# Performance work log

Measured on AMD Instinct MI355X. Metric: run time of the kernel, lower is better.

The kernel has to match this reference:

```python
import jax, jax.numpy as jnp
import numpy as np

TEMP = 0.5  # init temperature
EPS = 1e-12  # F.normalize eps


def setup_inputs() -> dict:
    key = jax.random.key(0)
    k1, k2 = jax.random.split(key)
    batch_embedding = jax.random.normal(k1, (4096, 256), dtype=jnp.float32)
    labels = jax.random.randint(k2, (4096,), 0, 512, dtype=jnp.int64)
    return {"batch_embedding": batch_embedding, "labels": labels}


def reference(batch_embedding, labels):
    n = labels.shape[0]
    dt = batch_embedding.dtype
    # row-normalize; cosine_similarity of normalized rows == norm @ norm.T
    nrm = jnp.linalg.norm(batch_embedding, axis=1, keepdims=True)
    norm = batch_embedding / jnp.maximum(nrm, EPS)
    sim = norm @ norm.T  # [n, n]
    mask = (labels[:, None] == labels[None, :]).astype(dt)  # same-label pairs (incl. diagonal)
    eye = jnp.eye(n, dtype=dt)
    exp_sim = jnp.exp(sim / TEMP) * (1.0 - eye)  # zero diagonal
    pos = mask * exp_sim
    neg_sum = jnp.sum(exp_sim - pos, axis=1)  # per-row negative sum
    ratio = pos / (pos + neg_sum[:, None])
    loss_mat = -jnp.log((1.0 - mask) + ratio + eye)
    nnz = jnp.count_nonzero(loss_mat).astype(dt)
    return jnp.sum(loss_mat) / nnz
```

## Files before the change

kernel.cpp:

```cpp
#include <hip/hip_runtime.h>
#include <hip/hip_bf16.h>


#define N_ROWS 4096
#define K_DIM  256

typedef __attribute__((ext_vector_type(8))) short short8;
typedef __attribute__((ext_vector_type(4))) float float4v;
typedef __attribute__((ext_vector_type(4))) float f4;

#define PK_OFF    0
#define PART_OFF  (N_ROWS * K_DIM * 2)
#define PART_SZ   (5 * 32 * N_ROWS)
#define ACC_OFF   (PART_OFF + PART_SZ * 4)

__global__ void normalize_kernel(const float* __restrict__ emb,
                                 short* __restrict__ pk,
                                 float* __restrict__ acc) {
    int tile = blockIdx.x, t = threadIdx.x;
    __shared__ float lds[16 * 256];
    __shared__ float sc[16];
    const f4* src = (const f4*)(emb + tile * 16 * 256);
    f4* dst4 = (f4*)lds;
    #pragma unroll
    for (int it = 0; it < 4; ++it) dst4[t + 256 * it] = src[t + 256 * it];
    __syncthreads();
    int wave = t >> 6, lane = t & 63;
    int row = wave * 4 + (lane >> 4);
    float s = 0.f;
    #pragma unroll
    for (int m = 0; m < 16; ++m) {
        float x = lds[row * 256 + (lane & 15) + 16 * m];
        s += x * x;
    }
    s += __shfl_xor(s, 1); s += __shfl_xor(s, 2);
    s += __shfl_xor(s, 4); s += __shfl_xor(s, 8);
    float scale = 1.0f / fmaxf(sqrtf(s), 1e-12f);
    if ((lane & 15) == 0) sc[row] = scale;
    __syncthreads();
    short out[16];
    #pragma unroll
    for (int u = 0; u < 16; ++u) {
        int p = t * 16 + u;
        int j = p & 7, r16 = (p >> 3) & 15, quad = (p >> 7) & 3, c = p >> 9;
        int k = quad * 8 + c * 32 + j;
        float v = lds[r16 * 256 + k] * sc[r16];
        __hip_bfloat16 b = __float2bfloat16(v);
        out[u] = *(short*)&b;
    }
    short* dst = pk + tile * 4096 + t * 16;
    *(short8*)dst = *(short8*)out;
    *(short8*)(dst + 8) = *(short8*)(out + 8);
    if (tile == 0 && t < 2) acc[t] = 0.0f;
}

__global__ __launch_bounds__(512, 4)
void negsum_kernel(const short* __restrict__ pk,
                   const int* __restrict__ labels,
                   float* __restrict__ part) {
    __shared__ short bs[8 * 4096];
    __shared__ int   labS[128];
    int t = threadIdx.x;
    int w = t >> 6, lane = t & 63;
    int row16 = lane & 15, quad = lane >> 4;
    int J = blockIdx.x & 31;
    int igroup = blockIdx.x >> 5;

    {
        const short8* src = (const short8*)(pk + J * 32768);
        short8* dst = (short8*)bs;
        #pragma unroll
        for (int it = 0; it < 8; ++it)
            dst[t + it * 512] = src[t + it * 512];
        if (t < 128) labS[t] = labels[J * 128 + t];
    }
    __syncthreads();

    short8 af[2][8];
    int istrip0 = igroup * 16 + w * 2;
    #pragma unroll
    for (int s = 0; s < 2; ++s) {
        const short* ap = pk + ((istrip0 + s) << 12) + lane * 8;
        #pragma unroll
        for (int c = 0; c < 8; ++c)
            af[s][c] = *(const short8*)(ap + (c << 9));
    }
    int irow[2][4], labi[2][4];
    #pragma unroll
    for (int s = 0; s < 2; ++s)
        #pragma unroll
        for (int r = 0; r < 4; ++r) {
            irow[s][r] = (istrip0 + s) * 16 + quad * 4 + r;
            labi[s][r] = labels[irow[s][r]];
        }

    float nacc[2][4] = {{0,0,0,0},{0,0,0,0}};
    float pe[2][4]   = {{0,0,0,0},{0,0,0,0}};
    float pe2[2][4]  = {{0,0,0,0},{0,0,0,0}};
    float ptt[2][4]  = {{0,0,0,0},{0,0,0,0}};
    float pc[2][4]   = {{0,0,0,0},{0,0,0,0}};

    for (int jt = 0; jt < 8; ++jt) {
        const short* bp = bs + (jt << 12) + lane * 8;
        float4v acc[2] = {{0.f,0.f,0.f,0.f},{0.f,0.f,0.f,0.f}};
        #pragma unroll
        for (int c = 0; c < 8; ++c) {
            short8 b = *(const short8*)(bp + (c << 9));
            acc[0] = __builtin_amdgcn_mfma_f32_16x16x32_bf16(af[0][c], b, acc[0], 0, 0, 0);
            acc[1] = __builtin_amdgcn_mfma_f32_16x16x32_bf16(af[1][c], b, acc[1], 0, 0, 0);
        }
        int j    = J * 128 + jt * 16 + row16;
        int labj = labS[jt * 16 + row16];
        #pragma unroll
        for (int s = 0; s < 2; ++s) {
            #pragma unroll
            for (int r = 0; r < 4; ++r) {
                float t2 = 2.0f * acc[s][r];
                float e  = __expf(t2);
                bool same = (labj == labi[s][r]);
                bool p    = same && (j != irow[s][r]);
                float m   = p ? 1.0f : 0.0f;
                nacc[s][r] += same ? 0.0f : e;
                pe[s][r]   = fmaf(m, e,      pe[s][r]);
                pe2[s][r]  = fmaf(m, e * e,  pe2[s][r]);
                ptt[s][r]  = fmaf(m, t2,     ptt[s][r]);
                pc[s][r]  += m;
            }
        }
    }

    #pragma unroll
    for (int s = 0; s < 2; ++s)
        #pragma unroll
        for (int r = 0; r < 4; ++r) {
            float v0 = nacc[s][r], v1 = pe[s][r], v2 = pe2[s][r];
            float v3 = ptt[s][r],  v4 = pc[s][r];
            #pragma unroll
            for (int m = 1; m < 16; m <<= 1) {
                v0 += __shfl_xor(v0, m); v1 += __shfl_xor(v1, m);
                v2 += __shfl_xor(v2, m); v3 += __shfl_xor(v3, m);
                v4 += __shfl_xor(v4, m);
            }
            if (row16 == 0) {
                int idx = J * N_ROWS + irow[s][r];
                part[0 * 32 * N_ROWS + idx] = v0;
                part[1 * 32 * N_ROWS + idx] = v1;
                part[2 * 32 * N_ROWS + idx] = v2;
                part[3 * 32 * N_ROWS + idx] = v3;
                part[4 * 32 * N_ROWS + idx] = v4;
            }
        }
}

__global__ void rowreduce_kernel(const float* __restrict__ part,
                                 float* __restrict__ acc) {
    int i = blockIdx.x * 256 + threadIdx.x;
    float n = 0.f, e1 = 0.f, e2 = 0.f, tt = 0.f, c = 0.f;
    for (int J = 0; J < 32; ++J) {
        int idx = J * N_ROWS + i;
        n  += part[0 * 32 * N_ROWS + idx];
        e1 += part[1 * 32 * N_ROWS + idx];
        e2 += part[2 * 32 * N_ROWS + idx];
        tt += part[3 * 32 * N_ROWS + idx];
        c  += part[4 * 32 * N_ROWS + idx];
    }
    float lsum = 0.f;
    if (c > 0.f) {
        float invn = 1.0f / n;
        lsum = c * logf(n) + e1 * invn - 0.5f * e2 * invn * invn - tt;
    }
    #pragma unroll
    for (int off = 32; off > 0; off >>= 1) {
        lsum += __shfl_down(lsum, off, 64);
        c    += __shfl_down(c,    off, 64);
    }
    __shared__ float sl[4], sc2[4];
    int wave = threadIdx.x >> 6, lane = threadIdx.x & 63;
    if (lane == 0) { sl[wave] = lsum; sc2[wave] = c; }
    __syncthreads();
    if (threadIdx.x == 0) {
        atomicAdd(&acc[0], sl[0] + sl[1] + sl[2] + sl[3]);
        atomicAdd(&acc[1], sc2[0] + sc2[1] + sc2[2] + sc2[3]);
    }
}

__global__ void div_kernel(const float* __restrict__ acc, float* __restrict__ out) {
    if (threadIdx.x == 0) out[0] = acc[0] / acc[1];
}

extern "C" void kernel_launch(void* const* d_in, const int* in_sizes, int n_in,
                              void* d_out, int out_size, void* d_ws, size_t ws_size,
                              hipStream_t stream) {
    const float* emb    = (const float*)d_in[0];
    const int*   labels = (const int*)d_in[1];
    float* out = (float*)d_out;
    char*  ws  = (char*)d_ws;

    short* pk   = (short*)(ws + PK_OFF);
    float* part = (float*)(ws + PART_OFF);
    float* acc  = (float*)(ws + ACC_OFF);

    normalize_kernel<<<N_ROWS / 16, 256, 0, stream>>>(emb, pk, acc);
    negsum_kernel<<<512, 512, 0, stream>>>(pk, labels, part);
    rowreduce_kernel<<<16, 256, 0, stream>>>(part, acc);
    div_kernel<<<1, 64, 0, stream>>>(acc, out);
}
```

Before: 83.16 us.

## Use per-wave 64x64 register tiles with direct global loads and column-wise reduction

The similarity kernel drops the LDS-staged B panel and instead has each wave compute a 64x64 output tile with 16 MFMA accumulators, loading A and B fragments straight from global memory. Partial sums are now reduced along the row axis per column, which uses the symmetry of the similarity matrix, and the loss drops the second-order e^2 correction term in favour of the exact pe/n form. This cuts the partial buffers from five to four and removes the block barrier, but it raises register pressure and relies on L2 for operand reuse instead of shared memory.

```diff
diff --git a/kernel.cpp b/kernel.cpp
--- a/kernel.cpp
+++ b/kernel.cpp
@@ -11,8 +11,7 @@
 
 #define PK_OFF    0
 #define PART_OFF  (N_ROWS * K_DIM * 2)
-#define PART_SZ   (5 * 32 * N_ROWS)
-#define ACC_OFF   (PART_OFF + PART_SZ * 4)
+#define ACC_OFF   (PART_OFF + 4 * 64 * N_ROWS * 4)
 
 __global__ void normalize_kernel(const float* __restrict__ emb,
                                  short* __restrict__ pk,
@@ -54,129 +53,114 @@
     if (tile == 0 && t < 2) acc[t] = 0.0f;
 }
 
-__global__ __launch_bounds__(512, 4)
+__global__ __launch_bounds__(256, 2)
 void negsum_kernel(const short* __restrict__ pk,
                    const int* __restrict__ labels,
                    float* __restrict__ part) {
-    __shared__ short bs[8 * 4096];
-    __shared__ int   labS[128];
-    int t = threadIdx.x;
-    int w = t >> 6, lane = t & 63;
-    int row16 = lane & 15, quad = lane >> 4;
-    int J = blockIdx.x & 31;
-    int igroup = blockIdx.x >> 5;
+    int w = threadIdx.x >> 6, lane = threadIdx.x & 63;
+    int lane16 = lane & 15, quad = lane >> 4;
+    int wid = blockIdx.x * 4 + w;
+    int i64 = wid >> 6, j64 = wid & 63;
+    int ibase = i64 * 64, jbase = j64 * 64;
 
-    {
-        const short8* src = (const short8*)(pk + J * 32768);
-        short8* dst = (short8*)bs;
+    int labi[16], labj[4];
+    #pragma unroll
+    for (int it = 0; it < 4; ++it)
         #pragma unroll
-        for (int it = 0; it < 8; ++it)
-            dst[t + it * 512] = src[t + it * 512];
-        if (t < 128) labS[t] = labels[J * 128 + t];
+        for (int r = 0; r < 4; ++r)
+            labi[it * 4 + r] = labels[ibase + it * 16 + quad * 4 + r];
+    #pragma unroll
+    for (int jt = 0; jt < 4; ++jt)
+        labj[jt] = labels[jbase + jt * 16 + lane16];
+
+    float4v acc[4][4];
+    #pragma unroll
+    for (int a = 0; a < 4; ++a)
+        #pragma unroll
+        for (int b = 0; b < 4; ++b)
+            acc[a][b] = (float4v){0.f, 0.f, 0.f, 0.f};
+
+    for (int c = 0; c < 8; ++c) {
+        short8 af[4], bf[4];
+        #pragma unroll
+        for (int it = 0; it < 4; ++it)
+            af[it] = *(const short8*)(pk + (((i64 * 4 + it) << 12) | (c << 9)) + lane * 8);
+        #pragma unroll
+        for (int jt = 0; jt < 4; ++jt)
+            bf[jt] = *(const short8*)(pk + (((j64 * 4 + jt) << 12) | (c << 9)) + lane * 8);
+        #pragma unroll
+        for (int it = 0; it < 4; ++it)
+            #pragma unroll
+            for (int jt = 0; jt < 4; ++jt)
+                acc[it][jt] = __builtin_amdgcn_mfma_f32_16x16x32_bf16(
+                    af[it], bf[jt], acc[it][jt], 0, 0, 0);
     }
-    __syncthreads();
 
-    short8 af[2][8];
-    int istrip0 = igroup * 16 + w * 2;
+    float ex[4] = {0,0,0,0}, pe[4] = {0,0,0,0};
+    float tt[4] = {0,0,0,0}, pc[4] = {0,0,0,0};
     #pragma unroll
-    for (int s = 0; s < 2; ++s) {
-        const short* ap = pk + ((istrip0 + s) << 12) + lane * 8;
+    for (int it = 0; it < 4; ++it) {
         #pragma unroll
-        for (int c = 0; c < 8; ++c)
-            af[s][c] = *(const short8*)(ap + (c << 9));
-    }
-    int irow[2][4], labi[2][4];
-    #pragma unroll
-    for (int s = 0; s < 2; ++s)
-        #pragma unroll
-        for (int r = 0; r < 4; ++r) {
-            irow[s][r] = (istrip0 + s) * 16 + quad * 4 + r;
-            labi[s][r] = labels[irow[s][r]];
-        }
-
-    float nacc[2][4] = {{0,0,0,0},{0,0,0,0}};
-    float pe[2][4]   = {{0,0,0,0},{0,0,0,0}};
-    float pe2[2][4]  = {{0,0,0,0},{0,0,0,0}};
-    float ptt[2][4]  = {{0,0,0,0},{0,0,0,0}};
-    float pc[2][4]   = {{0,0,0,0},{0,0,0,0}};
-
-    for (int jt = 0; jt < 8; ++jt) {
-        const short* bp = bs + (jt << 12) + lane * 8;
-        float4v acc[2] = {{0.f,0.f,0.f,0.f},{0.f,0.f,0.f,0.f}};
-        #pragma unroll
-        for (int c = 0; c < 8; ++c) {
-            short8 b = *(const short8*)(bp + (c << 9));
-            acc[0] = __builtin_amdgcn_mfma_f32_16x16x32_bf16(af[0][c], b, acc[0], 0, 0, 0);
-            acc[1] = __builtin_amdgcn_mfma_f32_16x16x32_bf16(af[1][c], b, acc[1], 0, 0, 0);
-        }
-        int j    = J * 128 + jt * 16 + row16;
-        int labj = labS[jt * 16 + row16];
-        #pragma unroll
-        for (int s = 0; s < 2; ++s) {
+        for (int jt = 0; jt < 4; ++jt) {
+            int j = jbase + jt * 16 + lane16;
             #pragma unroll
             for (int r = 0; r < 4; ++r) {
-                float t2 = 2.0f * acc[s][r];
+                int i = ibase + it * 16 + quad * 4 + r;
+                float t2 = 2.0f * acc[it][jt][r];
                 float e  = __expf(t2);
-                bool same = (labj == labi[s][r]);
-                bool p    = same && (j != irow[s][r]);
-                float m   = p ? 1.0f : 0.0f;
-                nacc[s][r] += same ? 0.0f : e;
-                pe[s][r]   = fmaf(m, e,      pe[s][r]);
-                pe2[s][r]  = fmaf(m, e * e,  pe2[s][r]);
-                ptt[s][r]  = fmaf(m, t2,     ptt[s][r]);
-                pc[s][r]  += m;
+                bool keep = (i != j);
+                bool same = (labi[it * 4 + r] == labj[jt]);
+                ex[jt] += keep ? e : 0.0f;
+                float m = (same && keep) ? 1.0f : 0.0f;
+                pe[jt] = fmaf(m, e,  pe[jt]);
+                tt[jt] = fmaf(m, t2, tt[jt]);
+                pc[jt] += m;
             }
         }
     }
 
     #pragma unroll
-    for (int s = 0; s < 2; ++s)
-        #pragma unroll
-        for (int r = 0; r < 4; ++r) {
-            float v0 = nacc[s][r], v1 = pe[s][r], v2 = pe2[s][r];
-            float v3 = ptt[s][r],  v4 = pc[s][r];
-            #pragma unroll
-            for (int m = 1; m < 16; m <<= 1) {
-                v0 += __shfl_xor(v0, m); v1 += __shfl_xor(v1, m);
-                v2 += __shfl_xor(v2, m); v3 += __shfl_xor(v3, m);
-                v4 += __shfl_xor(v4, m);
-            }
-            if (row16 == 0) {
-                int idx = J * N_ROWS + irow[s][r];
-                part[0 * 32 * N_ROWS + idx] = v0;
-                part[1 * 32 * N_ROWS + idx] = v1;
-                part[2 * 32 * N_ROWS + idx] = v2;
-                part[3 * 32 * N_ROWS + idx] = v3;
-                part[4 * 32 * N_ROWS + idx] = v4;
-            }
+    for (int jt = 0; jt < 4; ++jt) {
+        float v0 = ex[jt], v1 = pe[jt], v2 = tt[jt], v3 = pc[jt];
+        v0 += __shfl_xor(v0, 16); v0 += __shfl_xor(v0, 32);
+        v1 += __shfl_xor(v1, 16); v1 += __shfl_xor(v1, 32);
+        v2 += __shfl_xor(v2, 16); v2 += __shfl_xor(v2, 32);
+        v3 += __shfl_xor(v3, 16); v3 += __shfl_xor(v3, 32);
+        if (quad == 0) {
+            int col = jbase + jt * 16 + lane16;
+            part[((0 * 64 + i64) << 12) + col] = v0;
+            part[((1 * 64 + i64) << 12) + col] = v1;
+            part[((2 * 64 + i64) << 12) + col] = v2;
+            part[((3 * 64 + i64) << 12) + col] = v3;
         }
+    }
 }
 
 __global__ void rowreduce_kernel(const float* __restrict__ part,
                                  float* __restrict__ acc) {
-    int i = blockIdx.x * 256 + threadIdx.x;
-    float n = 0.f, e1 = 0.f, e2 = 0.f, tt = 0.f, c = 0.f;
-    for (int J = 0; J < 32; ++J) {
-        int idx = J * N_ROWS + i;
-        n  += part[0 * 32 * N_ROWS + idx];
-        e1 += part[1 * 32 * N_ROWS + idx];
-        e2 += part[2 * 32 * N_ROWS + idx];
-        tt += part[3 * 32 * N_ROWS + idx];
-        c  += part[4 * 32 * N_ROWS + idx];
+    int j = blockIdx.x * 256 + threadIdx.x;
+    float ex = 0.f, pe = 0.f, tt = 0.f, pc = 0.f;
+    for (int ch = 0; ch < 64; ++ch) {
+        ex += part[((0 * 64 + ch) << 12) + j];
+        pe += part[((1 * 64 + ch) << 12) + j];
+        tt += part[((2 * 64 + ch) << 12) + j];
+        pc += part[((3 * 64 + ch) << 12) + j];
     }
     float lsum = 0.f;
-    if (c > 0.f) {
-        float invn = 1.0f / n;
-        lsum = c * logf(n) + e1 * invn - 0.5f * e2 * invn * invn - tt;
+    if (pc > 0.f) {
+        float n = ex - pe;
+        lsum = pc * logf(n) + pe / n - tt;
+    } else {
+        pc = 0.f;
     }
     #pragma unroll
     for (int off = 32; off > 0; off >>= 1) {
         lsum += __shfl_down(lsum, off, 64);
-        c    += __shfl_down(c,    off, 64);
+        pc   += __shfl_down(pc,   off, 64);
     }
     __shared__ float sl[4], sc2[4];
     int wave = threadIdx.x >> 6, lane = threadIdx.x & 63;
-    if (lane == 0) { sl[wave] = lsum; sc2[wave] = c; }
+    if (lane == 0) { sl[wave] = lsum; sc2[wave] = pc; }
     __syncthreads();
     if (threadIdx.x == 0) {
         atomicAdd(&acc[0], sl[0] + sl[1] + sl[2] + sl[3]);
@@ -201,7 +185,7 @@
     float* acc  = (float*)(ws + ACC_OFF);
 
     normalize_kernel<<<N_ROWS / 16, 256, 0, stream>>>(emb, pk, acc);
-    negsum_kernel<<<512, 512, 0, stream>>>(pk, labels, part);
+    negsum_kernel<<<1024, 256, 0, stream>>>(pk, labels, part);
     rowreduce_kernel<<<16, 256, 0, stream>>>(part, acc);
     div_kernel<<<1, 64, 0, stream>>>(acc, out);
 }
```

After: 91.70 us. 1.1x slower.
